# Kernel optimization log

Hardware: AMD Instinct MI355X
Metric: run time of the kernel (lower is better)

## Reference

```python
import jax, jax.numpy as jnp
import numpy as np

N_EMBD = 768
N_HEAD = 12
DIM_HEAD = N_EMBD // N_HEAD


def setup_inputs() -> dict:
    key = jax.random.key(0)
    k1, k2, k3 = jax.random.split(key, 3)
    B, T = 4, 2048
    x = jax.random.normal(k1, (B, T, N_EMBD), dtype=jnp.float32)
    # torch Linear(n_embd, 3*n_embd, bias=False): y = x @ W.T, W:[3C,C].
    # Store pre-transposed [C,3C] for direct matmul.
    s = 1.0 / np.sqrt(N_EMBD)
    W_qkv = jax.random.uniform(k2, (N_EMBD, 3 * N_EMBD), dtype=jnp.float32, minval=-s, maxval=s)
    W_proj = jax.random.uniform(k3, (N_EMBD, N_EMBD), dtype=jnp.float32, minval=-s, maxval=s)
    return {"x": x, "W_qkv": W_qkv, "W_proj": W_proj}


def reference(x, W_qkv, W_proj):
    B, T, C = x.shape
    qkv = x @ W_qkv                                  # [B,T,3C]
    q, k, v = jnp.split(qkv, 3, axis=-1)
    def heads(t):  # [B,T,C] -> [B,H,T,Dh]
        return t.reshape(B, T, N_HEAD, DIM_HEAD).transpose(0, 2, 1, 3)
    q, k, v = heads(q), heads(k), heads(v)
    # Source divides by scale = dim_head**-0.5, i.e. multiplies by sqrt(dim_head).
    scores = jnp.einsum('bhtd,bhsd->bhts', q, k) * jnp.sqrt(jnp.float32(DIM_HEAD))
    attn = jax.nn.softmax(scores, axis=-1)           # [B,H,T,T] materialized
    y = jnp.einsum('bhts,bhsd->bhtd', attn, v)       # [B,H,T,Dh]
    y = y.transpose(0, 2, 1, 3).reshape(B, T, C)
    return y @ W_proj
```

## Files before the change

### kernel.cpp

```cpp
#include <hip/hip_runtime.h>

typedef _Float16 f16;
typedef f16 f16x4 __attribute__((ext_vector_type(4)));
typedef f16 f16x8 __attribute__((ext_vector_type(8)));
typedef __fp16 h16x2 __attribute__((ext_vector_type(2)));
typedef float floatx4 __attribute__((ext_vector_type(4)));

#define LDT 72
#define LDTV 136
#define QSCALE 11.5415603271117f

__global__ __launch_bounds__(256) void convert_f32_f16(const float* __restrict__ in,
                                                       f16* __restrict__ out, int n) {
  int i = (blockIdx.x * 256 + threadIdx.x) * 4;
  if (i >= n) return;
  float4 v = *(const float4*)(in + i);
  f16x4 o = {(f16)v.x, (f16)v.y, (f16)v.z, (f16)v.w};
  *(f16x4*)(out + i) = o;
}

__global__ __launch_bounds__(256) void transpose_f32_f16_tiled(const float* __restrict__ in,
                                                               f16* __restrict__ out,
                                                               int K, int N) {
  __shared__ f16 tile[64][LDT];
  int k0 = blockIdx.x * 64, n0 = blockIdx.y * 64;
  int tid = threadIdx.x;
  int r = tid >> 4, c4 = (tid & 15) * 4;
  for (int p = 0; p < 4; ++p) {
    int rr = r + p * 16;
    float4 v = *(const float4*)(in + (size_t)(k0 + rr) * N + n0 + c4);
    tile[c4 + 0][rr] = (f16)v.x;
    tile[c4 + 1][rr] = (f16)v.y;
    tile[c4 + 2][rr] = (f16)v.z;
    tile[c4 + 3][rr] = (f16)v.w;
  }
  __syncthreads();
  int rn = tid >> 3, ck = (tid & 7) * 8;
  for (int p = 0; p < 2; ++p) {
    int rr = rn + p * 32;
    *(uint4*)(out + (size_t)(n0 + rr) * K + k0 + ck) = *(const uint4*)(&tile[rr][ck]);
  }
}

__global__ __launch_bounds__(256) void gemm1_qkv(const f16* __restrict__ A,
                                                 const f16* __restrict__ Bt,
                                                 f16* __restrict__ q16, f16* __restrict__ k16,
                                                 f16* __restrict__ vt) {
  __shared__ f16 As[128 * LDT];
  __shared__ f16 Bs[128 * LDT];
  int tid = threadIdx.x;
  int lane = tid & 63, wid = tid >> 6;
  int quad = lane >> 4, l16 = lane & 15;
  int wy = wid >> 1, wx = wid & 1;
  int m0 = blockIdx.x * 128, n0 = blockIdx.y * 128;
  int srow = tid >> 3, scol = (tid & 7) * 8;
  floatx4 acc[4][4] = {};
  for (int k0 = 0; k0 < 768; k0 += 64) {
    for (int p = 0; p < 4; ++p) {
      int r = srow + p * 32;
      *(uint4*)(As + r * LDT + scol) = *(const uint4*)(A + (size_t)(m0 + r) * 768 + k0 + scol);
      *(uint4*)(Bs + r * LDT + scol) = *(const uint4*)(Bt + (size_t)(n0 + r) * 768 + k0 + scol);
    }
    __syncthreads();
    for (int kk = 0; kk < 64; kk += 32) {
      f16x8 af[4], bfr[4];
      for (int i = 0; i < 4; ++i)
        af[i] = *(const f16x8*)(As + (wy * 64 + i * 16 + l16) * LDT + kk + quad * 8);
      for (int j = 0; j < 4; ++j)
        bfr[j] = *(const f16x8*)(Bs + (wx * 64 + j * 16 + l16) * LDT + kk + quad * 8);
      for (int i = 0; i < 4; ++i)
        for (int j = 0; j < 4; ++j)
          acc[i][j] = __builtin_amdgcn_mfma_f32_16x16x32_f16(af[i], bfr[j], acc[i][j], 0, 0, 0);
    }
    __syncthreads();
  }
  for (int i = 0; i < 4; ++i)
    for (int j = 0; j < 4; ++j)
      for (int r = 0; r < 4; ++r) {
        int row = m0 + wy * 64 + i * 16 + quad * 4 + r;
        int col = n0 + wx * 64 + j * 16 + l16;
        float a = acc[i][j][r];
        int b = row >> 11, t = row & 2047;
        if (col < 768) {
          int h = col >> 6, d = col & 63;
          q16[((size_t)(b * 12 + h)) * 131072 + (size_t)t * 64 + d] = (f16)(a * QSCALE);
        } else if (col < 1536) {
          int c = col - 768;
          int h = c >> 6, d = c & 63;
          k16[((size_t)(b * 12 + h)) * 131072 + (size_t)t * 64 + d] = (f16)a;
        } else {
          int c = col - 1536;
          int h = c >> 6, d = c & 63;
          vt[((size_t)(b * 12 + h)) * 131072 + (size_t)d * 2048 + t] = (f16)a;
        }
      }
}

__global__ __launch_bounds__(256) void gemm_bt_f16(const f16* __restrict__ A,
                                                   const f16* __restrict__ Bt,
                                                   float* __restrict__ C,
                                                   int M, int N, int K) {
  __shared__ f16 As[128 * LDT];
  __shared__ f16 Bs[128 * LDT];
  int tid = threadIdx.x;
  int lane = tid & 63, wid = tid >> 6;
  int quad = lane >> 4, l16 = lane & 15;
  int wy = wid >> 1, wx = wid & 1;
  int m0 = blockIdx.x * 128, n0 = blockIdx.y * 128;
  int srow = tid >> 3, scol = (tid & 7) * 8;
  floatx4 acc[4][4] = {};
  for (int k0 = 0; k0 < K; k0 += 64) {
    for (int p = 0; p < 4; ++p) {
      int r = srow + p * 32;
      *(uint4*)(As + r * LDT + scol) = *(const uint4*)(A + (size_t)(m0 + r) * K + k0 + scol);
      *(uint4*)(Bs + r * LDT + scol) = *(const uint4*)(Bt + (size_t)(n0 + r) * K + k0 + scol);
    }
    __syncthreads();
    for (int kk = 0; kk < 64; kk += 32) {
      f16x8 af[4], bfr[4];
      for (int i = 0; i < 4; ++i)
        af[i] = *(const f16x8*)(As + (wy * 64 + i * 16 + l16) * LDT + kk + quad * 8);
      for (int j = 0; j < 4; ++j)
        bfr[j] = *(const f16x8*)(Bs + (wx * 64 + j * 16 + l16) * LDT + kk + quad * 8);
      for (int i = 0; i < 4; ++i)
        for (int j = 0; j < 4; ++j)
          acc[i][j] = __builtin_amdgcn_mfma_f32_16x16x32_f16(af[i], bfr[j], acc[i][j], 0, 0, 0);
    }
    __syncthreads();
  }
  for (int i = 0; i < 4; ++i) {
    int row = m0 + wy * 64 + i * 16 + quad * 4;
    for (int j = 0; j < 4; ++j) {
      int col = n0 + wx * 64 + j * 16 + l16;
      for (int r = 0; r < 4; ++r)
        C[(size_t)(row + r) * N + col] = acc[i][j][r];
    }
  }
}

__global__ __launch_bounds__(256, 2) void flash_attn(const f16* __restrict__ q16,
                                                     const f16* __restrict__ k16,
                                                     const f16* __restrict__ vT,
                                                     f16* __restrict__ y) {
  __shared__ f16 Ks[128 * LDT];
  __shared__ f16 Vt[64 * LDTV];
  const int T = 2048;
  int xcd = blockIdx.x & 7, yb = blockIdx.x >> 3;
  int bh = xcd * 6 + (yb >> 5);
  int qt = yb & 31;
  int b = bh / 12, h = bh - b * 12;
  int tid = threadIdx.x;
  int lane = tid & 63, wid = tid >> 6;
  int quad = lane >> 4, l16 = lane & 15;
  int rk = tid >> 3, ck = (tid & 7) * 8;
  int rv = tid >> 4, cv = (tid & 15) * 8;
  size_t hb = (size_t)bh * T * 64;

  f16x8 qf[2];
  {
    size_t qrow = hb + (size_t)(qt * 64 + wid * 16 + l16) * 64 + quad * 8;
    qf[0] = *(const f16x8*)(q16 + qrow);
    qf[1] = *(const f16x8*)(q16 + qrow + 32);
  }
  f16x4 ones4;
  for (int e = 0; e < 4; ++e) ones4[e] = (f16)1.0f;

  float m_i = -1e30f, l_i = 0.f;
  floatx4 o[4] = {};

  for (int kt = 0; kt < 16; ++kt) {
    if (kt) __syncthreads();
    for (int p = 0; p < 4; ++p) {
      int r = rk + p * 32;
      *(uint4*)(Ks + r * LDT + ck) =
          *(const uint4*)(k16 + hb + (size_t)(kt * 128 + r) * 64 + ck);
      int d = rv + p * 16;
      *(uint4*)(Vt + d * LDTV + cv) =
          *(const uint4*)(vT + hb + (size_t)d * T + kt * 128 + cv);
    }
    __syncthreads();

    floatx4 sf[8];
    const floatx4 z4 = {0.f, 0.f, 0.f, 0.f};
    for (int i = 0; i < 8; ++i) sf[i] = z4;
    for (int kk = 0; kk < 2; ++kk)
      for (int i = 0; i < 8; ++i) {
        f16x8 kf = *(const f16x8*)(Ks + (i * 16 + l16) * LDT + kk * 32 + quad * 8);
        sf[i] = __builtin_amdgcn_mfma_f32_16x16x32_f16(kf, qf[kk], sf[i], 0, 0, 0);
      }

    float mx = fmaxf(fmaxf(sf[0][0], sf[0][1]), fmaxf(sf[0][2], sf[0][3]));
    for (int i = 1; i < 8; ++i)
      mx = fmaxf(mx, fmaxf(fmaxf(sf[i][0], sf[i][1]), fmaxf(sf[i][2], sf[i][3])));
    mx = fmaxf(mx, __shfl_xor(mx, 16));
    mx = fmaxf(mx, __shfl_xor(mx, 32));
    float m_new = fmaxf(m_i, mx);
    float alpha = exp2f(m_i - m_new);
    m_i = m_new;
    for (int i = 0; i < 8; ++i)
      for (int r = 0; r < 4; ++r) sf[i][r] = exp2f(sf[i][r] - m_new);
    for (int i = 0; i < 4; ++i) o[i] *= alpha;

    f16x4 pf[8];
    for (int i = 0; i < 8; ++i) {
      union { h16x2 h; f16 f[2]; } lo, hi;
      lo.h = __builtin_amdgcn_cvt_pkrtz(sf[i][0], sf[i][1]);
      hi.h = __builtin_amdgcn_cvt_pkrtz(sf[i][2], sf[i][3]);
      pf[i][0] = lo.f[0]; pf[i][1] = lo.f[1];
      pf[i][2] = hi.f[0]; pf[i][3] = hi.f[1];
    }

    floatx4 rs = z4;
    for (int si = 0; si < 8; ++si)
      rs = __builtin_amdgcn_mfma_f32_16x16x16f16(ones4, pf[si], rs, 0, 0, 0);
    l_i = l_i * alpha + rs[0];

    for (int i = 0; i < 4; ++i)
      for (int si = 0; si < 8; ++si) {
        f16x4 vf = *(const f16x4*)(Vt + (i * 16 + l16) * LDTV + si * 16 + quad * 4);
        o[i] = __builtin_amdgcn_mfma_f32_16x16x16f16(vf, pf[si], o[i], 0, 0, 0);
      }
  }

  float invl = 1.0f / l_i;
  int t = qt * 64 + wid * 16 + l16;
  size_t off = ((size_t)(b * T + t)) * 768 + h * 64;
  for (int i = 0; i < 4; ++i)
    for (int r = 0; r < 4; ++r)
      y[off + i * 16 + quad * 4 + r] = (f16)(o[i][r] * invl);
}

extern "C" void kernel_launch(void* const* d_in, const int* in_sizes, int n_in,
                              void* d_out, int out_size, void* d_ws, size_t ws_size,
                              hipStream_t stream) {
  const float* x     = (const float*)d_in[0];
  const float* Wqkv  = (const float*)d_in[1];
  const float* Wproj = (const float*)d_in[2];
  float* out = (float*)d_out;
  char* ws = (char*)d_ws;
  f16* x16    = (f16*)ws;
  f16* q16    = (f16*)(ws + 12582912);
  f16* k16    = (f16*)(ws + 25165824);
  f16* vT16   = (f16*)(ws + 37748736);
  f16* y16    = (f16*)(ws + 50331648);
  f16* WqkvT  = (f16*)(ws + 62914560);
  f16* WprojT = (f16*)(ws + 66453504);

  convert_f32_f16<<<6144, 256, 0, stream>>>(x, x16, 6291456);
  transpose_f32_f16_tiled<<<dim3(12, 36), 256, 0, stream>>>(Wqkv, WqkvT, 768, 2304);
  transpose_f32_f16_tiled<<<dim3(12, 12), 256, 0, stream>>>(Wproj, WprojT, 768, 768);
  gemm1_qkv<<<dim3(64, 18), 256, 0, stream>>>(x16, WqkvT, q16, k16, vT16);
  flash_attn<<<1536, 256, 0, stream>>>(q16, k16, vT16, y16);
  gemm_bt_f16<<<dim3(64, 6), 256, 0, stream>>>(y16, WprojT, out, 8192, 768, 768);
}
```

Before: 275.1 us.

## Swizzle LDS tiles with XOR and compute softmax exponent in half precision

Replaces the padded shared-memory layouts (LDT/LDTV strides) with unpadded tiles using XOR chunk swizzles in both GEMMs and the flash-attention K/V tiles. The goal is to avoid LDS bank conflicts while saving shared memory. In the attention kernel, the score minus the row max is now converted to fp16 first and exponentiated in fp16 (packed exp2), which cuts fp32 transcendental work. The cost is accuracy: arguments and probabilities are rounded to half precision before the exponential.

```diff
diff --git a/kernel.cpp b/kernel.cpp
--- a/kernel.cpp
+++ b/kernel.cpp
@@ -6,9 +6,8 @@
 typedef __fp16 h16x2 __attribute__((ext_vector_type(2)));
 typedef float floatx4 __attribute__((ext_vector_type(4)));
 
-#define LDT 72
-#define LDTV 136
 #define QSCALE 11.5415603271117f
+
 
 __global__ __launch_bounds__(256) void convert_f32_f16(const float* __restrict__ in,
                                                        f16* __restrict__ out, int n) {
@@ -22,7 +21,7 @@
 __global__ __launch_bounds__(256) void transpose_f32_f16_tiled(const float* __restrict__ in,
                                                                f16* __restrict__ out,
                                                                int K, int N) {
-  __shared__ f16 tile[64][LDT];
+  __shared__ f16 tile[64][72];
   int k0 = blockIdx.x * 64, n0 = blockIdx.y * 64;
   int tid = threadIdx.x;
   int r = tid >> 4, c4 = (tid & 15) * 4;
@@ -46,28 +45,36 @@
                                                  const f16* __restrict__ Bt,
                                                  f16* __restrict__ q16, f16* __restrict__ k16,
                                                  f16* __restrict__ vt) {
-  __shared__ f16 As[128 * LDT];
-  __shared__ f16 Bs[128 * LDT];
+  __shared__ f16 As[128 * 64];
+  __shared__ f16 Bs[128 * 64];
   int tid = threadIdx.x;
   int lane = tid & 63, wid = tid >> 6;
   int quad = lane >> 4, l16 = lane & 15;
   int wy = wid >> 1, wx = wid & 1;
   int m0 = blockIdx.x * 128, n0 = blockIdx.y * 128;
-  int srow = tid >> 3, scol = (tid & 7) * 8;
+  int srow = tid >> 3;
+  int schunk = tid & 7;
+  int scol = schunk * 8;
+  int swz = (schunk ^ (srow & 7)) * 8;
   floatx4 acc[4][4] = {};
   for (int k0 = 0; k0 < 768; k0 += 64) {
     for (int p = 0; p < 4; ++p) {
       int r = srow + p * 32;
-      *(uint4*)(As + r * LDT + scol) = *(const uint4*)(A + (size_t)(m0 + r) * 768 + k0 + scol);
-      *(uint4*)(Bs + r * LDT + scol) = *(const uint4*)(Bt + (size_t)(n0 + r) * 768 + k0 + scol);
-    }
-    __syncthreads();
-    for (int kk = 0; kk < 64; kk += 32) {
+      *(uint4*)(As + r * 64 + swz) = *(const uint4*)(A + (size_t)(m0 + r) * 768 + k0 + scol);
+      *(uint4*)(Bs + r * 64 + swz) = *(const uint4*)(Bt + (size_t)(n0 + r) * 768 + k0 + scol);
+    }
+    __syncthreads();
+    for (int kk = 0; kk < 2; ++kk) {
+      int cch = kk * 4 + quad;
       f16x8 af[4], bfr[4];
-      for (int i = 0; i < 4; ++i)
-        af[i] = *(const f16x8*)(As + (wy * 64 + i * 16 + l16) * LDT + kk + quad * 8);
-      for (int j = 0; j < 4; ++j)
-        bfr[j] = *(const f16x8*)(Bs + (wx * 64 + j * 16 + l16) * LDT + kk + quad * 8);
+      for (int i = 0; i < 4; ++i) {
+        int row = wy * 64 + i * 16 + l16;
+        af[i] = *(const f16x8*)(As + row * 64 + ((cch ^ (l16 & 7)) * 8));
+      }
+      for (int j = 0; j < 4; ++j) {
+        int row = wx * 64 + j * 16 + l16;
+        bfr[j] = *(const f16x8*)(Bs + row * 64 + ((cch ^ (l16 & 7)) * 8));
+      }
       for (int i = 0; i < 4; ++i)
         for (int j = 0; j < 4; ++j)
           acc[i][j] = __builtin_amdgcn_mfma_f32_16x16x32_f16(af[i], bfr[j], acc[i][j], 0, 0, 0);
@@ -100,28 +107,36 @@
                                                    const f16* __restrict__ Bt,
                                                    float* __restrict__ C,
                                                    int M, int N, int K) {
-  __shared__ f16 As[128 * LDT];
-  __shared__ f16 Bs[128 * LDT];
+  __shared__ f16 As[128 * 64];
+  __shared__ f16 Bs[128 * 64];
   int tid = threadIdx.x;
   int lane = tid & 63, wid = tid >> 6;
   int quad = lane >> 4, l16 = lane & 15;
   int wy = wid >> 1, wx = wid & 1;
   int m0 = blockIdx.x * 128, n0 = blockIdx.y * 128;
-  int srow = tid >> 3, scol = (tid & 7) * 8;
+  int srow = tid >> 3;
+  int schunk = tid & 7;
+  int scol = schunk * 8;
+  int swz = (schunk ^ (srow & 7)) * 8;
   floatx4 acc[4][4] = {};
   for (int k0 = 0; k0 < K; k0 += 64) {
     for (int p = 0; p < 4; ++p) {
       int r = srow + p * 32;
-      *(uint4*)(As + r * LDT + scol) = *(const uint4*)(A + (size_t)(m0 + r) * K + k0 + scol);
-      *(uint4*)(Bs + r * LDT + scol) = *(const uint4*)(Bt + (size_t)(n0 + r) * K + k0 + scol);
-    }
-    __syncthreads();
-    for (int kk = 0; kk < 64; kk += 32) {
+      *(uint4*)(As + r * 64 + swz) = *(const uint4*)(A + (size_t)(m0 + r) * K + k0 + scol);
+      *(uint4*)(Bs + r * 64 + swz) = *(const uint4*)(Bt + (size_t)(n0 + r) * K + k0 + scol);
+    }
+    __syncthreads();
+    for (int kk = 0; kk < 2; ++kk) {
+      int cch = kk * 4 + quad;
       f16x8 af[4], bfr[4];
-      for (int i = 0; i < 4; ++i)
-        af[i] = *(const f16x8*)(As + (wy * 64 + i * 16 + l16) * LDT + kk + quad * 8);
-      for (int j = 0; j < 4; ++j)
-        bfr[j] = *(const f16x8*)(Bs + (wx * 64 + j * 16 + l16) * LDT + kk + quad * 8);
+      for (int i = 0; i < 4; ++i) {
+        int row = wy * 64 + i * 16 + l16;
+        af[i] = *(const f16x8*)(As + row * 64 + ((cch ^ (l16 & 7)) * 8));
+      }
+      for (int j = 0; j < 4; ++j) {
+        int row = wx * 64 + j * 16 + l16;
+        bfr[j] = *(const f16x8*)(Bs + row * 64 + ((cch ^ (l16 & 7)) * 8));
+      }
       for (int i = 0; i < 4; ++i)
         for (int j = 0; j < 4; ++j)
           acc[i][j] = __builtin_amdgcn_mfma_f32_16x16x32_f16(af[i], bfr[j], acc[i][j], 0, 0, 0);
@@ -142,8 +157,8 @@
                                                      const f16* __restrict__ k16,
                                                      const f16* __restrict__ vT,
                                                      f16* __restrict__ y) {
-  __shared__ f16 Ks[128 * LDT];
-  __shared__ f16 Vt[64 * LDTV];
+  __shared__ f16 Ks[128 * 64];
+  __shared__ f16 Vt[64 * 128];
   const int T = 2048;
   int xcd = blockIdx.x & 7, yb = blockIdx.x >> 3;
   int bh = xcd * 6 + (yb >> 5);
@@ -152,8 +167,10 @@
   int tid = threadIdx.x;
   int lane = tid & 63, wid = tid >> 6;
   int quad = lane >> 4, l16 = lane & 15;
-  int rk = tid >> 3, ck = (tid & 7) * 8;
-  int rv = tid >> 4, cv = (tid & 15) * 8;
+  int rk = tid >> 3, kch = tid & 7;
+  int rv = tid >> 4, vch = tid & 15;
+  int kswz = (kch ^ (rk & 7)) * 8;
+  int vswz = (vch ^ rv) * 8;
   size_t hb = (size_t)bh * T * 64;
 
   f16x8 qf[2];
@@ -172,11 +189,11 @@
     if (kt) __syncthreads();
     for (int p = 0; p < 4; ++p) {
       int r = rk + p * 32;
-      *(uint4*)(Ks + r * LDT + ck) =
-          *(const uint4*)(k16 + hb + (size_t)(kt * 128 + r) * 64 + ck);
+      *(uint4*)(Ks + r * 64 + kswz) =
+          *(const uint4*)(k16 + hb + (size_t)(kt * 128 + r) * 64 + kch * 8);
       int d = rv + p * 16;
-      *(uint4*)(Vt + d * LDTV + cv) =
-          *(const uint4*)(vT + hb + (size_t)d * T + kt * 128 + cv);
+      *(uint4*)(Vt + d * 128 + vswz) =
+          *(const uint4*)(vT + hb + (size_t)d * T + kt * 128 + vch * 8);
     }
     __syncthreads();
 
@@ -185,7 +202,8 @@
     for (int i = 0; i < 8; ++i) sf[i] = z4;
     for (int kk = 0; kk < 2; ++kk)
       for (int i = 0; i < 8; ++i) {
-        f16x8 kf = *(const f16x8*)(Ks + (i * 16 + l16) * LDT + kk * 32 + quad * 8);
+        int row = i * 16 + l16;
+        f16x8 kf = *(const f16x8*)(Ks + row * 64 + (((kk * 4 + quad) ^ (l16 & 7)) * 8));
         sf[i] = __builtin_amdgcn_mfma_f32_16x16x32_f16(kf, qf[kk], sf[i], 0, 0, 0);
       }
 
@@ -197,17 +215,19 @@
     float m_new = fmaxf(m_i, mx);
     float alpha = exp2f(m_i - m_new);
     m_i = m_new;
-    for (int i = 0; i < 8; ++i)
-      for (int r = 0; r < 4; ++r) sf[i][r] = exp2f(sf[i][r] - m_new);
     for (int i = 0; i < 4; ++i) o[i] *= alpha;
 
     f16x4 pf[8];
     for (int i = 0; i < 8; ++i) {
-      union { h16x2 h; f16 f[2]; } lo, hi;
-      lo.h = __builtin_amdgcn_cvt_pkrtz(sf[i][0], sf[i][1]);
-      hi.h = __builtin_amdgcn_cvt_pkrtz(sf[i][2], sf[i][3]);
-      pf[i][0] = lo.f[0]; pf[i][1] = lo.f[1];
-      pf[i][2] = hi.f[0]; pf[i][3] = hi.f[1];
+      union { h16x2 h; f16 f[2]; } a2, b2;
+      a2.h = __builtin_amdgcn_cvt_pkrtz(sf[i][0] - m_new, sf[i][1] - m_new);
+      b2.h = __builtin_amdgcn_cvt_pkrtz(sf[i][2] - m_new, sf[i][3] - m_new);
+      f16x4 uu = {a2.f[0], a2.f[1], b2.f[0], b2.f[1]};
+#if __has_builtin(__builtin_elementwise_exp2)
+      pf[i] = __builtin_elementwise_exp2(uu);
+#else
+      for (int r = 0; r < 4; ++r) pf[i][r] = (f16)exp2f((float)uu[r]);
+#endif
     }
 
     floatx4 rs = z4;
@@ -217,7 +237,9 @@
 
     for (int i = 0; i < 4; ++i)
       for (int si = 0; si < 8; ++si) {
-        f16x4 vf = *(const f16x4*)(Vt + (i * 16 + l16) * LDTV + si * 16 + quad * 4);
+        int d = i * 16 + l16;
+        int cch = si * 2 + (quad >> 1);
+        f16x4 vf = *(const f16x4*)(Vt + d * 128 + ((cch ^ l16) * 8) + (quad & 1) * 4);
         o[i] = __builtin_amdgcn_mfma_f32_16x16x16f16(vf, pf[si], o[i], 0, 0, 0);
       }
   }
```

Result: slower. 285.3 us (+3.7%).
